# Optimization experiments

Hardware: AMD Instinct MI355X
Metric: run time of the kernel (lower is better)

Reference implementation:

```python
import jax, jax.numpy as jnp
import numpy as np

IN_C, OUT_C, K, UP, C_DIM = 128, 64, 3, 2, 512
CLAMP = 256.0
ACT_GAIN = np.sqrt(2.0)  # lrelu def_gain


def _upfirdn_up2(x, f2):
    """upfirdn2d with up=2, padding=(3,2,3,2), gain=up^2 for a 4-tap filter.

    Padding values come from conv2d_resample: p = k//2 = 1, fw = 4, up = 2 =>
    px0 = p + (fw+up-1)//2 = 3, px1 = p + (fw-up)//2 = 2.
    """
    N, C, H, W = x.shape
    px0, px1 = 3, 2
    # zero-insert upsample (interior padding) fused with edge padding;
    # trailing zero of the up-sampled signal folded into the high pad.
    x = jax.lax.pad(x, jnp.asarray(0, x.dtype),
                    ((0, 0, 0), (0, 0, 0),
                     (px0, px1 + (UP - 1), UP - 1),
                     (px0, px1 + (UP - 1), UP - 1)))
    k = (f2 * (UP * UP)).astype(x.dtype)[None, None]   # [1,1,4,4], symmetric -> flip is a no-op
    k = jnp.tile(k, (C, 1, 1, 1))                       # depthwise FIR
    return jax.lax.conv_general_dilated(
        x, k, window_strides=(1, 1), padding='VALID',
        feature_group_count=C, dimension_numbers=('NCHW', 'OIHW', 'NCHW'))


def setup_inputs() -> dict:
    key = jax.random.key(0)
    ks = jax.random.split(key, 4)
    return {
        "x": jax.random.normal(ks[0], (8, IN_C, 128, 128), jnp.float32),
        "c": jax.random.normal(ks[1], (8, C_DIM), jnp.float32),
        "weight": jax.random.normal(ks[2], (OUT_C, IN_C, K, K), jnp.float32),
        "bias": jnp.zeros((OUT_C,), jnp.float32),
        "w_affine": jax.random.normal(ks[3], (IN_C, C_DIM), jnp.float32),
        "b_affine": jnp.zeros((IN_C,), jnp.float32),
    }


def reference(x, c, weight, bias, w_affine, b_affine):
    # setup_filter: normalize separable FIR taps
    f1 = jnp.array([1.0, 3.0, 3.0, 1.0], jnp.float32)
    f1 = f1 / jnp.sum(f1)
    f2 = jnp.outer(f1, f1)

    # hyper modulation: x *= 1 + tanh(affine(c))
    y = c @ (w_affine * (1.0 / np.sqrt(C_DIM))).T + b_affine   # FullyConnectedLayer, linear
    x = x * (1.0 + jnp.tanh(y))[:, :, None, None]

    # conv2d_resample(up=2, padding=k//2, flip_weight=False)
    w = weight * (1.0 / np.sqrt(IN_C * K * K))                  # weight_gain
    x = _upfirdn_up2(x, f2)                                      # [N,C,2H+2,2W+2]
    w = w[:, :, ::-1, ::-1]                                      # flip_weight=False => true convolution
    x = jax.lax.conv_general_dilated(
        x, w.astype(x.dtype), window_strides=(1, 1), padding='VALID',
        dimension_numbers=('NCHW', 'OIHW', 'NCHW'))              # [N,OUT_C,2H,2W]

    # bias_act: lrelu(x+b)*sqrt(2), clamp at +-256 (gain=1)
    x = jax.nn.leaky_relu(x + bias[None, :, None, None], 0.2) * ACT_GAIN
    return jnp.clip(x, -CLAMP, CLAMP)
```

## Files before the change

### kernel.cpp

```cpp
#include <hip/hip_runtime.h>
#include <math.h>

#define IN_C   128
#define OUT_C  64
#define CDIM   512
#define HW     128
#define PHW    130
#define OHW    256
#define NB     8

typedef __attribute__((ext_vector_type(8))) short short8;
typedef __attribute__((ext_vector_type(4))) float f32x4;

__device__ inline unsigned short f2bf(float f) {
    unsigned int u = __float_as_uint(f);
    unsigned int r = (u + 0x7fffu + ((u >> 16) & 1u)) >> 16;
    return (unsigned short)r;
}

__device__ inline float postact(float v) {
    v = v > 0.f ? v : 0.2f * v;
    v *= 1.4142135623730951f;
    return fminf(fmaxf(v, -256.f), 256.f);
}

__device__ __forceinline__ void gload16(const void* g, void* l) {
    __builtin_amdgcn_global_load_lds(
        (const __attribute__((address_space(1))) unsigned int*)g,
        (__attribute__((address_space(3))) unsigned int*)l, 16, 0, 0);
}

__global__ void gain_kernel(const float* __restrict__ c,
                            const float* __restrict__ w_affine,
                            const float* __restrict__ b_affine,
                            float* __restrict__ gain) {
    int wave = (blockIdx.x * blockDim.x + threadIdx.x) >> 6;
    int lane = threadIdx.x & 63;
    if (wave >= NB * IN_C) return;
    int n  = wave >> 7;
    int ic = wave & 127;
    const float* cp = c + n * CDIM;
    const float* wp = w_affine + ic * CDIM;
    float s = 0.f;
    #pragma unroll
    for (int k = 0; k < CDIM / 64; ++k) s += cp[lane + 64 * k] * wp[lane + 64 * k];
    #pragma unroll
    for (int off = 32; off > 0; off >>= 1) s += __shfl_down(s, off);
    if (lane == 0) {
        float y = s * 0.04419417382415922f + b_affine[ic];
        gain[n * IN_C + ic] = 1.0f + tanhf(y);
    }
}

__global__ void wbprep2_kernel(const float* __restrict__ w, unsigned short* __restrict__ wb2) {
    int idx = blockIdx.x * blockDim.x + threadIdx.x;
    if (idx >= 18 * 16384) return;
    int e    = idx & 7;
    int lane = (idx >> 3) & 63;
    int m16  = (idx >> 9) & 15;
    int kc   = (idx >> 13) & 1;
    int kt   = idx >> 14;
    int tap = kt >> 1, h = kt & 1;
    int m  = m16 * 16 + (lane & 15);
    int ic = h * 64 + kc * 32 + (lane >> 4) * 8 + e;
    int ky = tap / 3, kx = tap % 3;
    int oc = m >> 2, ph = m & 3;
    int py = ph >> 1, px = ph & 1;
    int sy = 2 * ky + (py == 0 ? 1 : 0);
    int sx = 2 * kx + (px == 0 ? 1 : 0);
    const float k1[4] = {0.25f, 0.75f, 0.75f, 0.25f};
    float sum = 0.f;
    #pragma unroll
    for (int by = 0; by < 3; ++by) {
        int ay = sy - by;
        if (ay < 0 || ay > 3) continue;
        #pragma unroll
        for (int bx = 0; bx < 3; ++bx) {
            int ax = sx - bx;
            if (ax < 0 || ax > 3) continue;
            sum += w[((oc * IN_C + ic) * 3 + (2 - by)) * 3 + (2 - bx)] * k1[ay] * k1[ax];
        }
    }
    wb2[idx] = f2bf(sum * 0.029462782549439483f);
}

__global__ __launch_bounds__(256) void xprep_kernel(const float* __restrict__ x,
                                                    const float* __restrict__ gain,
                                                    unsigned short* __restrict__ xg) {
    int n = blockIdx.x >> 7;
    int y = blockIdx.x & 127;
    __shared__ unsigned short lds[128][130];
    int tid = threadIdx.x;
    for (int i = tid; i < 128 * 128; i += 256) {
        int ic = i >> 7, pix = i & 127;
        float v = x[(((n * IN_C + ic) * HW) + y) * HW + pix] * gain[n * IN_C + ic];
        lds[pix][ic] = f2bf(v);
    }
    __syncthreads();
    unsigned int* dst = (unsigned int*)(xg + (((size_t)(n * PHW) + y + 1) * PHW + 1) * 128);
    for (int i = tid; i < 8192; i += 256) {
        int pix = i >> 6, d = i & 63;
        int j = d >> 2, w = d & 3;
        int js = j ^ ((pix + 1) & 7);
        dst[pix * 64 + js * 4 + w] = *reinterpret_cast<const unsigned int*>(&lds[pix][d * 2]);
    }
}

__global__ void border_kernel(unsigned short* __restrict__ xg) {
    int id = blockIdx.x * blockDim.x + threadIdx.x;
    int c = id & 15;
    int t = id >> 4;
    int p = t % 516;
    int n = t / 516;
    if (n >= NB) return;
    int Y, X;
    if (p < 130)      { Y = 0;   X = p; }
    else if (p < 260) { Y = 129; X = p - 130; }
    else              { int q = p - 260; Y = 1 + (q >> 1); X = (q & 1) * 129; }
    uint4 z = make_uint4(0, 0, 0, 0);
    *reinterpret_cast<uint4*>(xg + (((size_t)(n * PHW) + Y) * PHW + X) * 128 + c * 8) = z;
}

#define BARRIER() do { __builtin_amdgcn_sched_barrier(0); __builtin_amdgcn_s_barrier(); __builtin_amdgcn_sched_barrier(0); } while (0)
#define MM(ACC, AF, BF) ACC = __builtin_amdgcn_mfma_f32_16x16x32_bf16(AF, BF, ACC, 0, 0, 0)

__global__ __launch_bounds__(512) void conv_mfma3(
    const unsigned short* __restrict__ xg,
    const unsigned short* __restrict__ wb2,
    const float* __restrict__ bias,
    float* __restrict__ out) {
    __shared__ __align__(16) char smem[148480];

    const int bid   = blockIdx.x;
    const int n     = bid >> 6;
    const int patch = bid & 63;
    const int Y0 = (patch >> 3) * 16;
    const int X0 = (patch & 7) * 16;
    const int tid  = threadIdx.x;
    const int lane = tid & 63;
    const int wid  = tid >> 6;
    const int wM = wid >> 2;
    const int wN = wid & 3;
    const int l16 = lane & 15;
    const int lhi = lane >> 4;
    const int mbase = wM * 8;
    const int pbase = wN * 4;

    const char* xgb  = (const char*)xg + (size_t)n * PHW * PHW * 256;
    const char* wb2b = (const char*)wb2;

    #pragma unroll 1
    for (int i = 0; i < 11; ++i) {
        int c = i * 512 + tid;
        if (c < 5184) {
            int r = c / 288;
            int t = c - r * 288;
            gload16(xgb + ((size_t)(Y0 + r) * PHW + X0) * 256 + t * 16,
                    smem + 65536 + (i * 512 + wid * 64) * 16);
        }
    }

    auto stageA = [&](int k, int p) {
        const char* aS = wb2b + k * 32768;
        char* buf = smem + (p << 15);
        #pragma unroll
        for (int r = 0; r < 4; ++r)
            gload16(aS + (r * 512 + tid) * 16, buf + (r * 512 + wid * 64) * 16);
    };

    f32x4 acc[8][4];
    #pragma unroll
    for (int f = 0; f < 8; ++f)
        #pragma unroll
        for (int b = 0; b < 4; ++b) acc[f][b] = (f32x4)0.f;

    stageA(0, 0);
    stageA(1, 1);

    #pragma unroll 1
    for (int t = 0; t < 18; ++t) {
        const int p   = t & 1;
        const int tap = t >> 1;
        const int h   = t & 1;
        const int ky  = tap / 3;
        const int kx  = tap - ky * 3;
        const char* bA = smem + (p << 15);

        if (t < 17) { asm volatile("s_waitcnt vmcnt(4)" ::: "memory"); }
        else        { asm volatile("s_waitcnt vmcnt(0)" ::: "memory"); }
        BARRIER();

        auto ldA = [&](int f, int kc) -> short8 {
            return *reinterpret_cast<const short8*>(bA + (((kc << 4) + mbase + f) << 10) + (lane << 4));
        };
        auto ldB = [&](int b, int kc) -> short8 {
            int R = pbase + b + ky;
            int C = l16 + kx;
            int icoff = (h << 7) + (kc << 6) + (lhi << 4);
            return *reinterpret_cast<const short8*>(
                smem + 65536 + (R * 18 + C) * 256 + (icoff ^ ((C & 7) << 4)));
        };

        #pragma unroll
        for (int kc = 0; kc < 2; ++kc) {
            short8 Af[8], Bf[4];
            #pragma unroll
            for (int f = 0; f < 8; ++f) Af[f] = ldA(f, kc);
            #pragma unroll
            for (int b = 0; b < 4; ++b) Bf[b] = ldB(b, kc);
            __builtin_amdgcn_s_setprio(1);
            #pragma unroll
            for (int f = 0; f < 8; ++f)
                #pragma unroll
                for (int b = 0; b < 4; ++b) MM(acc[f][b], Af[f], Bf[b]);
            __builtin_amdgcn_s_setprio(0);
        }

        BARRIER();
        if (t + 2 < 18) stageA(t + 2, p);
    }

    #pragma unroll
    for (int f = 0; f < 8; ++f) {
        const int oc = wM * 32 + f * 4 + lhi;
        const float bi = bias[oc];
        #pragma unroll
        for (int b = 0; b < 4; ++b) {
            const int ypix = Y0 + pbase + b;
            const int xpix = X0 + l16;
            float* o0 = out + (((size_t)(n * OUT_C + oc) * OHW) + 2 * ypix) * OHW + 2 * xpix;
            float2 v0 = make_float2(postact(acc[f][b][0] + bi), postact(acc[f][b][1] + bi));
            float2 v1 = make_float2(postact(acc[f][b][2] + bi), postact(acc[f][b][3] + bi));
            *reinterpret_cast<float2*>(o0) = v0;
            *reinterpret_cast<float2*>(o0 + OHW) = v1;
        }
    }
}

__global__ void wprep_kernel(const float* __restrict__ w, float* __restrict__ wp) {
    int idx = blockIdx.x * blockDim.x + threadIdx.x;
    if (idx >= IN_C * 9 * 4 * OUT_C) return;
    int oc = idx & 63;
    int t  = idx >> 6;
    int ph = t & 3;  t >>= 2;
    int kx = t % 3;  t /= 3;
    int ky = t % 3;  t /= 3;
    int ic = t;
    int py = ph >> 1, px = ph & 1;
    int sy = 2 * ky + (py == 0 ? 1 : 0);
    int sx = 2 * kx + (px == 0 ? 1 : 0);
    const float k1[4] = {0.25f, 0.75f, 0.75f, 0.25f};
    float sum = 0.f;
    #pragma unroll
    for (int by = 0; by < 3; ++by) {
        int ay = sy - by;
        if (ay < 0 || ay > 3) continue;
        #pragma unroll
        for (int bx = 0; bx < 3; ++bx) {
            int ax = sx - bx;
            if (ax < 0 || ax > 3) continue;
            sum += w[((oc * IN_C + ic) * 3 + (2 - by)) * 3 + (2 - bx)] * k1[ay] * k1[ax];
        }
    }
    wp[idx] = sum * 0.029462782549439483f;
}

__global__ __launch_bounds__(256) void conv_main(
    const float* __restrict__ x, const float* __restrict__ gain,
    const float* __restrict__ wp, const float* __restrict__ bias,
    float* __restrict__ out) {
    const int n    = blockIdx.z >> 3;
    const int occ  = (blockIdx.z & 7) * 8;
    const int tx0  = blockIdx.x * 16;
    const int ty0  = blockIdx.y * 16;
    const int tid  = threadIdx.x;
    const int lx   = tid & 15;
    const int ly   = tid >> 4;
    __shared__ float xsf[8][18][18];
    float acc[4][8];
    #pragma unroll
    for (int p = 0; p < 4; ++p)
        #pragma unroll
        for (int o = 0; o < 8; ++o) acc[p][o] = 0.f;
    for (int ic0 = 0; ic0 < IN_C; ic0 += 8) {
        __syncthreads();
        for (int i = tid; i < 8 * 324; i += 256) {
            int icb = i / 324;
            int rem = i - icb * 324;
            int yy  = rem / 18;
            int xx  = rem - yy * 18;
            int gy  = ty0 + yy - 1;
            int gx  = tx0 + xx - 1;
            int ic  = ic0 + icb;
            float v = 0.f;
            if (gy >= 0 && gy < HW && gx >= 0 && gx < HW)
                v = x[((n * IN_C + ic) * HW + gy) * HW + gx] * gain[n * IN_C + ic];
            xsf[icb][yy][xx] = v;
        }
        __syncthreads();
        for (int icb = 0; icb < 8; ++icb) {
            const int ic = ic0 + icb;
            const float* wpp = wp + ic * (9 * 4 * OUT_C) + occ;
            #pragma unroll
            for (int ky = 0; ky < 3; ++ky)
                #pragma unroll
                for (int kx = 0; kx < 3; ++kx) {
                    float tv = xsf[icb][ly + ky][lx + kx];
                    const float* w9 = wpp + (ky * 3 + kx) * (4 * OUT_C);
                    #pragma unroll
                    for (int p = 0; p < 4; ++p)
                        #pragma unroll
                        for (int o = 0; o < 8; ++o)
                            acc[p][o] = fmaf(tv, w9[p * OUT_C + o], acc[p][o]);
                }
        }
    }
    const int ybase = 2 * (ty0 + ly);
    const int xbase = 2 * (tx0 + lx);
    #pragma unroll
    for (int o = 0; o < 8; ++o) {
        float b = bias[occ + o];
        #pragma unroll
        for (int py = 0; py < 2; ++py) {
            float2 v;
            v.x = postact(acc[py * 2 + 0][o] + b);
            v.y = postact(acc[py * 2 + 1][o] + b);
            *reinterpret_cast<float2*>(
                &out[((size_t)(n * OUT_C + occ + o) * OHW + (ybase + py)) * OHW + xbase]) = v;
        }
    }
}

extern "C" void kernel_launch(void* const* d_in, const int* in_sizes, int n_in,
                              void* d_out, int out_size, void* d_ws, size_t ws_size,
                              hipStream_t stream) {
    const float* x        = (const float*)d_in[0];
    const float* c        = (const float*)d_in[1];
    const float* weight   = (const float*)d_in[2];
    const float* bias     = (const float*)d_in[3];
    const float* w_affine = (const float*)d_in[4];
    const float* b_affine = (const float*)d_in[5];
    float* out = (float*)d_out;

    float* gain = (float*)d_ws;

    const size_t NEED = 1048576 + (size_t)NB * PHW * PHW * IN_C * 2;
    if (ws_size >= NEED) {
        unsigned short* wb2 = (unsigned short*)((char*)d_ws + 8192);
        unsigned short* xg  = (unsigned short*)((char*)d_ws + 1048576);
        gain_kernel<<<dim3((NB * IN_C * 64) / 256), dim3(256), 0, stream>>>(c, w_affine, b_affine, gain);
        wbprep2_kernel<<<dim3((18 * 16384) / 256), dim3(256), 0, stream>>>(weight, wb2);
        xprep_kernel<<<dim3(NB * HW), dim3(256), 0, stream>>>(x, gain, xg);
        border_kernel<<<dim3((NB * 516 * 16) / 256), dim3(256), 0, stream>>>(xg);
        conv_mfma3<<<dim3(512), dim3(512), 0, stream>>>(xg, wb2, bias, out);
    } else {
        float* wp = (float*)((char*)d_ws + 8192);
        gain_kernel<<<dim3((NB * IN_C * 64) / 256), dim3(256), 0, stream>>>(c, w_affine, b_affine, gain);
        wprep_kernel<<<dim3((IN_C * 9 * 4 * OUT_C + 255) / 256), dim3(256), 0, stream>>>(weight, wp);
        conv_main<<<dim3(HW / 16, HW / 16, NB * 8), dim3(256), 0, stream>>>(x, gain, wp, bias, out);
    }
}
```

Measured before the change: 111.6 us.

## Merge prep kernels and split conv K-step into quarter phases with finer A prefetch

Fuses the gain, weight-repack and border-zeroing kernels into one launch, which removes two kernel launches. It also rewrites the conv main loop so each K step runs in four phases, with half-tile A loads staged between them and smaller register fragments. The weight layout is regrouped to match, blocks are remapped so neighbouring blocks span different batches, and launch_bounds requests 2 waves per EU. The intent is better load/compute overlap and lower register pressure, at the cost of more barriers per step.

```diff
diff --git a/kernel.cpp b/kernel.cpp
--- a/kernel.cpp
+++ b/kernel.cpp
@@ -28,6 +28,259 @@
     __builtin_amdgcn_global_load_lds(
         (const __attribute__((address_space(1))) unsigned int*)g,
         (__attribute__((address_space(3))) unsigned int*)l, 16, 0, 0);
+}
+
+__global__ __launch_bounds__(256) void prep_kernel(
+    const float* __restrict__ w, unsigned short* __restrict__ wb2,
+    unsigned short* __restrict__ xg,
+    const float* __restrict__ c, const float* __restrict__ wa,
+    const float* __restrict__ ba, float* __restrict__ gain) {
+    int blk = blockIdx.x;
+    if (blk < 1152) {
+        int idx  = blk * 256 + threadIdx.x;
+        int e    = idx & 7;
+        int lane = (idx >> 3) & 63;
+        int pr   = (idx >> 9) & 31;
+        int kt   = idx >> 14;
+        int hh = pr >> 4, kcb = (pr >> 3) & 1, wM = (pr >> 2) & 1, fi = pr & 3;
+        int m   = (wM * 8 + hh * 4 + fi) * 16 + (lane & 15);
+        int ic  = (kt & 1) * 64 + kcb * 32 + (lane >> 4) * 8 + e;
+        int tap = kt >> 1;
+        int ky = tap / 3, kx = tap % 3;
+        int oc = m >> 2, ph = m & 3;
+        int py = ph >> 1, px = ph & 1;
+        int sy = 2 * ky + (py == 0 ? 1 : 0);
+        int sx = 2 * kx + (px == 0 ? 1 : 0);
+        const float k1[4] = {0.25f, 0.75f, 0.75f, 0.25f};
+        float sum = 0.f;
+        #pragma unroll
+        for (int by = 0; by < 3; ++by) {
+            int ay = sy - by;
+            if (ay < 0 || ay > 3) continue;
+            #pragma unroll
+            for (int bx = 0; bx < 3; ++bx) {
+                int ax = sx - bx;
+                if (ax < 0 || ax > 3) continue;
+                sum += w[((oc * IN_C + ic) * 3 + (2 - by)) * 3 + (2 - bx)] * k1[ay] * k1[ax];
+            }
+        }
+        wb2[idx] = f2bf(sum * 0.029462782549439483f);
+    } else if (blk < 1410) {
+        int id = (blk - 1152) * 256 + threadIdx.x;
+        int cc = id & 15;
+        int t  = id >> 4;
+        int p  = t % 516;
+        int n  = t / 516;
+        int Y, X;
+        if (p < 130)      { Y = 0;   X = p; }
+        else if (p < 260) { Y = 129; X = p - 130; }
+        else              { int q = p - 260; Y = 1 + (q >> 1); X = (q & 1) * 129; }
+        uint4 z = make_uint4(0, 0, 0, 0);
+        *reinterpret_cast<uint4*>(xg + (((size_t)(n * PHW) + Y) * PHW + X) * 128 + cc * 8) = z;
+    } else {
+        int wave = (blk - 1410) * 4 + (threadIdx.x >> 6);
+        int lane = threadIdx.x & 63;
+        int n  = wave >> 7;
+        int ic = wave & 127;
+        const float* cp = c + n * CDIM;
+        const float* wp = wa + ic * CDIM;
+        float s = 0.f;
+        #pragma unroll
+        for (int k = 0; k < CDIM / 64; ++k) s += cp[lane + 64 * k] * wp[lane + 64 * k];
+        #pragma unroll
+        for (int off = 32; off > 0; off >>= 1) s += __shfl_down(s, off);
+        if (lane == 0) {
+            float y = s * 0.04419417382415922f + ba[ic];
+            gain[n * IN_C + ic] = 1.0f + tanhf(y);
+        }
+    }
+}
+
+__global__ __launch_bounds__(256) void xprep_kernel(const float* __restrict__ x,
+                                                    const float* __restrict__ gain,
+                                                    unsigned short* __restrict__ xg) {
+    int n = blockIdx.x >> 7;
+    int y = blockIdx.x & 127;
+    __shared__ unsigned short lds[128][130];
+    int tid = threadIdx.x;
+    for (int i = tid; i < 128 * 128; i += 256) {
+        int ic = i >> 7, pix = i & 127;
+        float v = x[(((n * IN_C + ic) * HW) + y) * HW + pix] * gain[n * IN_C + ic];
+        lds[pix][ic] = f2bf(v);
+    }
+    __syncthreads();
+    unsigned int* dst = (unsigned int*)(xg + (((size_t)(n * PHW) + y + 1) * PHW + 1) * 128);
+    for (int i = tid; i < 8192; i += 256) {
+        int pix = i >> 6, d = i & 63;
+        int j = d >> 2, ww = d & 3;
+        int js = j ^ ((pix + 1) & 7);
+        dst[pix * 64 + js * 4 + ww] = *reinterpret_cast<const unsigned int*>(&lds[pix][d * 2]);
+    }
+}
+
+#define BARRIER() do { __builtin_amdgcn_sched_barrier(0); __builtin_amdgcn_s_barrier(); __builtin_amdgcn_sched_barrier(0); } while (0)
+#define MM(ACC, AF, BF) ACC = __builtin_amdgcn_mfma_f32_16x16x32_bf16(AF, BF, ACC, 0, 0, 0)
+
+__global__ __launch_bounds__(512, 2) void conv_mfma4(
+    const unsigned short* __restrict__ xg,
+    const unsigned short* __restrict__ wb2,
+    const float* __restrict__ bias,
+    float* __restrict__ out) {
+    __shared__ __align__(16) char smem[148480];
+
+    const int bid = blockIdx.x;
+    const int wg  = ((bid & 7) << 6) + (bid >> 3);
+    const int n     = wg >> 6;
+    const int patch = wg & 63;
+    const int Y0 = (patch >> 3) * 16;
+    const int X0 = (patch & 7) * 16;
+    const int tid  = threadIdx.x;
+    const int lane = tid & 63;
+    const int wid  = tid >> 6;
+    const int wM = wid >> 2;
+    const int wN = wid & 3;
+    const int l16 = lane & 15;
+    const int lhi = lane >> 4;
+    const int pbase = wN * 4;
+
+    const char* xgb = (const char*)xg + (size_t)n * PHW * PHW * 256;
+    const char* wbb = (const char*)wb2;
+    char* haloB = smem + 65536;
+
+    #pragma unroll 1
+    for (int i = 0; i < 11; ++i) {
+        int cc = i * 512 + tid;
+        if (cc < 5184) {
+            int r = cc / 288;
+            int t2 = cc - r * 288;
+            gload16(xgb + ((size_t)(Y0 + r) * PHW + X0) * 256 + t2 * 16,
+                    haloB + (i * 512 + wid * 64) * 16);
+        }
+    }
+
+    auto stageA = [&](int k, int hh, int half) {
+        gload16(wbb + k * 32768 + hh * 16384 + half * 8192 + tid * 16,
+                smem + ((k & 1) << 15) + hh * 16384 + half * 8192 + wid * 1024);
+    };
+
+    f32x4 acc[8][4];
+    #pragma unroll
+    for (int f = 0; f < 8; ++f)
+        #pragma unroll
+        for (int b = 0; b < 4; ++b) acc[f][b] = (f32x4)0.f;
+
+    stageA(0, 0, 0); stageA(0, 0, 1);
+    stageA(0, 1, 0); stageA(0, 1, 1);
+    stageA(1, 0, 0); stageA(1, 0, 1);
+    asm volatile("s_waitcnt vmcnt(4)" ::: "memory");
+    BARRIER();
+
+    #pragma unroll 1
+    for (int t = 0; t < 18; ++t) {
+        const char* bA = smem + ((t & 1) << 15);
+        const int tap = t >> 1;
+        const int h   = t & 1;
+        const int ky  = tap / 3;
+        const int kx  = tap - ky * 3;
+        const int C   = l16 + kx;
+        const int bswz = (C & 7) << 4;
+
+        auto ldB1 = [&](int b, int kc) -> short8 {
+            int icoff = ((h << 7) + (kc << 6) + (lhi << 4)) ^ bswz;
+            return *reinterpret_cast<const short8*>(
+                haloB + ((pbase + b + ky) * 18 + C) * 256 + icoff);
+        };
+
+        short8 Af[8], Bf0[4], Bf1[4];
+
+        #pragma unroll
+        for (int f = 0; f < 4; ++f)
+            #pragma unroll
+            for (int kc = 0; kc < 2; ++kc)
+                Af[f * 2 + kc] = *reinterpret_cast<const short8*>(
+                    bA + ((kc * 8 + wM * 4 + f) << 10) + (lane << 4));
+        #pragma unroll
+        for (int b = 0; b < 2; ++b)
+            #pragma unroll
+            for (int kc = 0; kc < 2; ++kc) Bf0[b * 2 + kc] = ldB1(b, kc);
+        if (t + 1 < 18) stageA(t + 1, 1, 0);
+        BARRIER();
+        __builtin_amdgcn_s_setprio(1);
+        #pragma unroll
+        for (int f = 0; f < 4; ++f)
+            #pragma unroll
+            for (int b = 0; b < 2; ++b) {
+                MM(acc[f][b], Af[f * 2 + 0], Bf0[b * 2 + 0]);
+                MM(acc[f][b], Af[f * 2 + 1], Bf0[b * 2 + 1]);
+            }
+        __builtin_amdgcn_s_setprio(0);
+
+        #pragma unroll
+        for (int b = 0; b < 2; ++b)
+            #pragma unroll
+            for (int kc = 0; kc < 2; ++kc) Bf1[b * 2 + kc] = ldB1(b + 2, kc);
+        if (t + 1 < 18) stageA(t + 1, 1, 1);
+        if (t < 17) { asm volatile("s_waitcnt vmcnt(4)" ::: "memory"); }
+        else        { asm volatile("s_waitcnt vmcnt(0)" ::: "memory"); }
+        BARRIER();
+        __builtin_amdgcn_s_setprio(1);
+        #pragma unroll
+        for (int f = 0; f < 4; ++f)
+            #pragma unroll
+            for (int b = 0; b < 2; ++b) {
+                MM(acc[f][b + 2], Af[f * 2 + 0], Bf1[b * 2 + 0]);
+                MM(acc[f][b + 2], Af[f * 2 + 1], Bf1[b * 2 + 1]);
+            }
+        __builtin_amdgcn_s_setprio(0);
+
+        #pragma unroll
+        for (int f = 0; f < 4; ++f)
+            #pragma unroll
+            for (int kc = 0; kc < 2; ++kc)
+                Af[f * 2 + kc] = *reinterpret_cast<const short8*>(
+                    bA + ((16 + kc * 8 + wM * 4 + f) << 10) + (lane << 4));
+        if (t + 2 < 18) stageA(t + 2, 0, 0);
+        BARRIER();
+        __builtin_amdgcn_s_setprio(1);
+        #pragma unroll
+        for (int f = 0; f < 4; ++f)
+            #pragma unroll
+            for (int b = 0; b < 2; ++b) {
+                MM(acc[4 + f][b], Af[f * 2 + 0], Bf0[b * 2 + 0]);
+                MM(acc[4 + f][b], Af[f * 2 + 1], Bf0[b * 2 + 1]);
+            }
+        __builtin_amdgcn_s_setprio(0);
+
+        if (t + 2 < 18) stageA(t + 2, 0, 1);
+        if (t < 16)       { asm volatile("s_waitcnt vmcnt(4)" ::: "memory"); }
+        else if (t == 16) { asm volatile("s_waitcnt vmcnt(2)" ::: "memory"); }
+        BARRIER();
+        __builtin_amdgcn_s_setprio(1);
+        #pragma unroll
+        for (int f = 0; f < 4; ++f)
+            #pragma unroll
+            for (int b = 0; b < 2; ++b) {
+                MM(acc[4 + f][b + 2], Af[f * 2 + 0], Bf1[b * 2 + 0]);
+                MM(acc[4 + f][b + 2], Af[f * 2 + 1], Bf1[b * 2 + 1]);
+            }
+        __builtin_amdgcn_s_setprio(0);
+    }
+
+    #pragma unroll
+    for (int f = 0; f < 8; ++f) {
+        const int oc = wM * 32 + f * 4 + lhi;
+        const float bi = bias[oc];
+        #pragma unroll
+        for (int b = 0; b < 4; ++b) {
+            const int ypix = Y0 + pbase + b;
+            const int xpix = X0 + l16;
+            float* o0 = out + (((size_t)(n * OUT_C + oc) * OHW) + 2 * ypix) * OHW + 2 * xpix;
+            float2 v0 = make_float2(postact(acc[f][b][0] + bi), postact(acc[f][b][1] + bi));
+            float2 v1 = make_float2(postact(acc[f][b][2] + bi), postact(acc[f][b][3] + bi));
+            *reinterpret_cast<float2*>(o0) = v0;
+            *reinterpret_cast<float2*>(o0 + OHW) = v1;
+        }
+    }
 }
 
 __global__ void gain_kernel(const float* __restrict__ c,
@@ -49,191 +302,6 @@
     if (lane == 0) {
         float y = s * 0.04419417382415922f + b_affine[ic];
         gain[n * IN_C + ic] = 1.0f + tanhf(y);
-    }
-}
-
-__global__ void wbprep2_kernel(const float* __restrict__ w, unsigned short* __restrict__ wb2) {
-    int idx = blockIdx.x * blockDim.x + threadIdx.x;
-    if (idx >= 18 * 16384) return;
-    int e    = idx & 7;
-    int lane = (idx >> 3) & 63;
-    int m16  = (idx >> 9) & 15;
-    int kc   = (idx >> 13) & 1;
-    int kt   = idx >> 14;
-    int tap = kt >> 1, h = kt & 1;
-    int m  = m16 * 16 + (lane & 15);
-    int ic = h * 64 + kc * 32 + (lane >> 4) * 8 + e;
-    int ky = tap / 3, kx = tap % 3;
-    int oc = m >> 2, ph = m & 3;
-    int py = ph >> 1, px = ph & 1;
-    int sy = 2 * ky + (py == 0 ? 1 : 0);
-    int sx = 2 * kx + (px == 0 ? 1 : 0);
-    const float k1[4] = {0.25f, 0.75f, 0.75f, 0.25f};
-    float sum = 0.f;
-    #pragma unroll
-    for (int by = 0; by < 3; ++by) {
-        int ay = sy - by;
-        if (ay < 0 || ay > 3) continue;
-        #pragma unroll
-        for (int bx = 0; bx < 3; ++bx) {
-            int ax = sx - bx;
-            if (ax < 0 || ax > 3) continue;
-            sum += w[((oc * IN_C + ic) * 3 + (2 - by)) * 3 + (2 - bx)] * k1[ay] * k1[ax];
-        }
-    }
-    wb2[idx] = f2bf(sum * 0.029462782549439483f);
-}
-
-__global__ __launch_bounds__(256) void xprep_kernel(const float* __restrict__ x,
-                                                    const float* __restrict__ gain,
-                                                    unsigned short* __restrict__ xg) {
-    int n = blockIdx.x >> 7;
-    int y = blockIdx.x & 127;
-    __shared__ unsigned short lds[128][130];
-    int tid = threadIdx.x;
-    for (int i = tid; i < 128 * 128; i += 256) {
-        int ic = i >> 7, pix = i & 127;
-        float v = x[(((n * IN_C + ic) * HW) + y) * HW + pix] * gain[n * IN_C + ic];
-        lds[pix][ic] = f2bf(v);
-    }
-    __syncthreads();
-    unsigned int* dst = (unsigned int*)(xg + (((size_t)(n * PHW) + y + 1) * PHW + 1) * 128);
-    for (int i = tid; i < 8192; i += 256) {
-        int pix = i >> 6, d = i & 63;
-        int j = d >> 2, w = d & 3;
-        int js = j ^ ((pix + 1) & 7);
-        dst[pix * 64 + js * 4 + w] = *reinterpret_cast<const unsigned int*>(&lds[pix][d * 2]);
-    }
-}
-
-__global__ void border_kernel(unsigned short* __restrict__ xg) {
-    int id = blockIdx.x * blockDim.x + threadIdx.x;
-    int c = id & 15;
-    int t = id >> 4;
-    int p = t % 516;
-    int n = t / 516;
-    if (n >= NB) return;
-    int Y, X;
-    if (p < 130)      { Y = 0;   X = p; }
-    else if (p < 260) { Y = 129; X = p - 130; }
-    else              { int q = p - 260; Y = 1 + (q >> 1); X = (q & 1) * 129; }
-    uint4 z = make_uint4(0, 0, 0, 0);
-    *reinterpret_cast<uint4*>(xg + (((size_t)(n * PHW) + Y) * PHW + X) * 128 + c * 8) = z;
-}
-
-#define BARRIER() do { __builtin_amdgcn_sched_barrier(0); __builtin_amdgcn_s_barrier(); __builtin_amdgcn_sched_barrier(0); } while (0)
-#define MM(ACC, AF, BF) ACC = __builtin_amdgcn_mfma_f32_16x16x32_bf16(AF, BF, ACC, 0, 0, 0)
-
-__global__ __launch_bounds__(512) void conv_mfma3(
-    const unsigned short* __restrict__ xg,
-    const unsigned short* __restrict__ wb2,
-    const float* __restrict__ bias,
-    float* __restrict__ out) {
-    __shared__ __align__(16) char smem[148480];
-
-    const int bid   = blockIdx.x;
-    const int n     = bid >> 6;
-    const int patch = bid & 63;
-    const int Y0 = (patch >> 3) * 16;
-    const int X0 = (patch & 7) * 16;
-    const int tid  = threadIdx.x;
-    const int lane = tid & 63;
-    const int wid  = tid >> 6;
-    const int wM = wid >> 2;
-    const int wN = wid & 3;
-    const int l16 = lane & 15;
-    const int lhi = lane >> 4;
-    const int mbase = wM * 8;
-    const int pbase = wN * 4;
-
-    const char* xgb  = (const char*)xg + (size_t)n * PHW * PHW * 256;
-    const char* wb2b = (const char*)wb2;
-
-    #pragma unroll 1
-    for (int i = 0; i < 11; ++i) {
-        int c = i * 512 + tid;
-        if (c < 5184) {
-            int r = c / 288;
-            int t = c - r * 288;
-            gload16(xgb + ((size_t)(Y0 + r) * PHW + X0) * 256 + t * 16,
-                    smem + 65536 + (i * 512 + wid * 64) * 16);
-        }
-    }
-
-    auto stageA = [&](int k, int p) {
-        const char* aS = wb2b + k * 32768;
-        char* buf = smem + (p << 15);
-        #pragma unroll
-        for (int r = 0; r < 4; ++r)
-            gload16(aS + (r * 512 + tid) * 16, buf + (r * 512 + wid * 64) * 16);
-    };
-
-    f32x4 acc[8][4];
-    #pragma unroll
-    for (int f = 0; f < 8; ++f)
-        #pragma unroll
-        for (int b = 0; b < 4; ++b) acc[f][b] = (f32x4)0.f;
-
-    stageA(0, 0);
-    stageA(1, 1);
-
-    #pragma unroll 1
-    for (int t = 0; t < 18; ++t) {
-        const int p   = t & 1;
-        const int tap = t >> 1;
-        const int h   = t & 1;
-        const int ky  = tap / 3;
-        const int kx  = tap - ky * 3;
-        const char* bA = smem + (p << 15);
-
-        if (t < 17) { asm volatile("s_waitcnt vmcnt(4)" ::: "memory"); }
-        else        { asm volatile("s_waitcnt vmcnt(0)" ::: "memory"); }
-        BARRIER();
-
-        auto ldA = [&](int f, int kc) -> short8 {
-            return *reinterpret_cast<const short8*>(bA + (((kc << 4) + mbase + f) << 10) + (lane << 4));
-        };
-        auto ldB = [&](int b, int kc) -> short8 {
-            int R = pbase + b + ky;
-            int C = l16 + kx;
-            int icoff = (h << 7) + (kc << 6) + (lhi << 4);
-            return *reinterpret_cast<const short8*>(
-                smem + 65536 + (R * 18 + C) * 256 + (icoff ^ ((C & 7) << 4)));
-        };
-
-        #pragma unroll
-        for (int kc = 0; kc < 2; ++kc) {
-            short8 Af[8], Bf[4];
-            #pragma unroll
-            for (int f = 0; f < 8; ++f) Af[f] = ldA(f, kc);
-            #pragma unroll
-            for (int b = 0; b < 4; ++b) Bf[b] = ldB(b, kc);
-            __builtin_amdgcn_s_setprio(1);
-            #pragma unroll
-            for (int f = 0; f < 8; ++f)
-                #pragma unroll
-                for (int b = 0; b < 4; ++b) MM(acc[f][b], Af[f], Bf[b]);
-            __builtin_amdgcn_s_setprio(0);
-        }
-
-        BARRIER();
-        if (t + 2 < 18) stageA(t + 2, p);
-    }
-
-    #pragma unroll
-    for (int f = 0; f < 8; ++f) {
-        const int oc = wM * 32 + f * 4 + lhi;
-        const float bi = bias[oc];
-        #pragma unroll
-        for (int b = 0; b < 4; ++b) {
-            const int ypix = Y0 + pbase + b;
-            const int xpix = X0 + l16;
-            float* o0 = out + (((size_t)(n * OUT_C + oc) * OHW) + 2 * ypix) * OHW + 2 * xpix;
-            float2 v0 = make_float2(postact(acc[f][b][0] + bi), postact(acc[f][b][1] + bi));
-            float2 v1 = make_float2(postact(acc[f][b][2] + bi), postact(acc[f][b][3] + bi));
-            *reinterpret_cast<float2*>(o0) = v0;
-            *reinterpret_cast<float2*>(o0 + OHW) = v1;
-        }
     }
 }
 
@@ -348,11 +416,9 @@
     if (ws_size >= NEED) {
         unsigned short* wb2 = (unsigned short*)((char*)d_ws + 8192);
         unsigned short* xg  = (unsigned short*)((char*)d_ws + 1048576);
-        gain_kernel<<<dim3((NB * IN_C * 64) / 256), dim3(256), 0, stream>>>(c, w_affine, b_affine, gain);
-        wbprep2_kernel<<<dim3((18 * 16384) / 256), dim3(256), 0, stream>>>(weight, wb2);
+        prep_kernel<<<dim3(1666), dim3(256), 0, stream>>>(weight, wb2, xg, c, w_affine, b_affine, gain);
         xprep_kernel<<<dim3(NB * HW), dim3(256), 0, stream>>>(x, gain, xg);
-        border_kernel<<<dim3((NB * 516 * 16) / 256), dim3(256), 0, stream>>>(xg);
-        conv_mfma3<<<dim3(512), dim3(512), 0, stream>>>(xg, wb2, bias, out);
+        conv_mfma4<<<dim3(512), dim3(512), 0, stream>>>(xg, wb2, bias, out);
     } else {
         float* wp = (float*)((char*)d_ws + 8192);
         gain_kernel<<<dim3((NB * IN_C * 64) / 256), dim3(256), 0, stream>>>(c, w_affine, b_affine, gain);
```

New measurement: 105.1 us. 1.06x faster.
